# Optimization experiments

Measured on AMD Instinct MI355X. Metric: run time of the kernel, lower is better.

The kernel has to match this reference:

```python
import jax, jax.numpy as jnp
import numpy as np

B, S, D = 32, 1024, 512
MAX_DUR = 8  # randint upper bound; after clamp durations lie in [1, MAX_DUR-1]


def setup_inputs() -> dict:
    key = jax.random.key(0)
    kx, kd = jax.random.split(key)
    x = jax.random.normal(kx, (B, S, D), dtype=jnp.float32)
    durations = jax.random.randint(kd, (B, S), 0, MAX_DUR).astype(jnp.int64)
    return {"x": x, "durations": durations}


def reference(x, durations):
    # torch: durations.long().clamp(min=1); per-batch repeat_interleave then
    # pad_sequence to the max expanded length across the batch.
    dur = jnp.clip(durations.astype(jnp.int32), 1, None)          # [B,S]
    cum = jnp.cumsum(dur, axis=1)                                  # [B,S] exclusive-right boundaries
    totals = cum[:, -1]                                            # [B] expanded lengths
    # pad_sequence pads to max total length across the batch; this is
    # intrinsically data-dependent, so concretize it eagerly.
    max_len = int(jnp.max(totals))
    pos = jnp.arange(max_len)                                      # [T]
    # token index for output frame t: smallest s with cum[s] > t
    idx = jax.vmap(lambda c: jnp.searchsorted(c, pos, side='right'))(cum)  # [B,T]
    idx = jnp.minimum(idx, S - 1)
    out = jnp.take_along_axis(x, idx[:, :, None], axis=1)          # [B,T,D] fused gather
    mask = (pos[None, :] < totals[:, None]).astype(x.dtype)        # zero the ragged tail
    return out * mask[:, :, None]
```

## Files before the change

kernel.cpp:

```cpp
#include <hip/hip_runtime.h>
#include <hip/hip_bf16.h>


constexpr int B = 32;
constexpr int S = 1024;
constexpr int D = 512;
constexpr int VEC = D / 4;
constexpr int BPB = 64;
constexpr int MAX_RPB = 128;

using f4 = __attribute__((ext_vector_type(4))) float;

__global__ void lr_fused(const int* __restrict__ durations,
                         const f4* __restrict__ x4,
                         f4* __restrict__ out,
                         int max_len) {
    const int b   = blockIdx.x >> 6;
    const int blk = blockIdx.x & (BPB - 1);
    const int rpb = (max_len + BPB - 1) / BPB;
    const int p0  = blk * rpb;
    const int p1  = min(p0 + rpb, max_len);
    if (p0 >= p1) return;

    const int t    = threadIdx.x;
    const int lane = t & 63;
    const int wv   = t >> 6;

    __shared__ int wsum[4];
    __shared__ int s_idx[MAX_RPB];

    int4 d4 = reinterpret_cast<const int4*>(durations + b * S)[t];
    const int d0 = d4.x < 1 ? 1 : d4.x;
    const int d1 = d4.y < 1 ? 1 : d4.y;
    const int d2 = d4.z < 1 ? 1 : d4.z;
    const int d3 = d4.w < 1 ? 1 : d4.w;
    const int tsum = d0 + d1 + d2 + d3;

    int inc = tsum;
    #pragma unroll
    for (int off = 1; off < 64; off <<= 1) {
        int n = __shfl_up(inc, off, 64);
        if (lane >= off) inc += n;
    }
    if (lane == 63) wsum[wv] = inc;

    const int nblk = p1 - p0;
    for (int q = t; q < nblk; q += 256) s_idx[q] = -1;
    __syncthreads();

    int base = 0;
    #pragma unroll
    for (int j = 0; j < 4; ++j) if (j < wv) base += wsum[j];

    int p = base + inc - tsum;
    int src = b * S + t * 4;
    {
        int e;
        e = p + d0; for (int q = max(p, p0); q < min(e, p1); ++q) s_idx[q - p0] = src; p = e; ++src;
        e = p + d1; for (int q = max(p, p0); q < min(e, p1); ++q) s_idx[q - p0] = src; p = e; ++src;
        e = p + d2; for (int q = max(p, p0); q < min(e, p1); ++q) s_idx[q - p0] = src; p = e; ++src;
        e = p + d3; for (int q = max(p, p0); q < min(e, p1); ++q) s_idx[q - p0] = src;
    }
    __syncthreads();

    const int qr = (nblk + 3) >> 2;
    int r  = wv * qr;
    int r1 = min(r + qr, nblk);

    f4* __restrict__ dbase = out + ((size_t)b * max_len + p0) * VEC;

    for (; r + 4 <= r1; r += 4) {
        const int i0 = __builtin_amdgcn_readfirstlane(s_idx[r]);
        const int i1 = __builtin_amdgcn_readfirstlane(s_idx[r + 1]);
        const int i2 = __builtin_amdgcn_readfirstlane(s_idx[r + 2]);
        const int i3 = __builtin_amdgcn_readfirstlane(s_idx[r + 3]);

        f4 a0 = {0,0,0,0}, c0 = {0,0,0,0};
        f4 a1 = {0,0,0,0}, c1 = {0,0,0,0};
        f4 a2 = {0,0,0,0}, c2 = {0,0,0,0};
        f4 a3 = {0,0,0,0}, c3 = {0,0,0,0};
        if (i0 >= 0) { const f4* s = x4 + (size_t)i0 * VEC; a0 = s[lane]; c0 = s[lane + 64]; }
        if (i1 >= 0) { const f4* s = x4 + (size_t)i1 * VEC; a1 = s[lane]; c1 = s[lane + 64]; }
        if (i2 >= 0) { const f4* s = x4 + (size_t)i2 * VEC; a2 = s[lane]; c2 = s[lane + 64]; }
        if (i3 >= 0) { const f4* s = x4 + (size_t)i3 * VEC; a3 = s[lane]; c3 = s[lane + 64]; }

        f4* __restrict__ d = dbase + (size_t)r * VEC;
        __builtin_nontemporal_store(a0, d + lane);
        __builtin_nontemporal_store(c0, d + lane + 64);
        __builtin_nontemporal_store(a1, d + VEC + lane);
        __builtin_nontemporal_store(c1, d + VEC + lane + 64);
        __builtin_nontemporal_store(a2, d + 2 * VEC + lane);
        __builtin_nontemporal_store(c2, d + 2 * VEC + lane + 64);
        __builtin_nontemporal_store(a3, d + 3 * VEC + lane);
        __builtin_nontemporal_store(c3, d + 3 * VEC + lane + 64);
    }
    for (; r < r1; ++r) {
        const int i0 = __builtin_amdgcn_readfirstlane(s_idx[r]);
        f4 a = {0,0,0,0}, c = {0,0,0,0};
        if (i0 >= 0) { const f4* s = x4 + (size_t)i0 * VEC; a = s[lane]; c = s[lane + 64]; }
        f4* __restrict__ d = dbase + (size_t)r * VEC;
        __builtin_nontemporal_store(a, d + lane);
        __builtin_nontemporal_store(c, d + lane + 64);
    }
}

extern "C" void kernel_launch(void* const* d_in, const int* in_sizes, int n_in,
                              void* d_out, int out_size, void* d_ws, size_t ws_size,
                              hipStream_t stream) {
    const float* x = (const float*)d_in[0];
    const int* durations = (const int*)d_in[1];
    float* out = (float*)d_out;

    const int max_len = out_size / (B * D);

    lr_fused<<<B * BPB, 256, 0, stream>>>(
        durations, (const f4*)x, (f4*)out, max_len);
}
```

Measured before the change: 55.10 us.

## Use 1024-thread blocks with one token per thread and fewer blocks per batch

Blocks per batch drop from 64 to 16 and block size grows from 256 to 1024 threads. Each thread now scans a single duration instead of four, and sixteen waves split the gather rows. The change cuts the number of blocks that each redo the full 1024-token prefix scan, so less scan work is repeated per output row. In exchange blocks are larger and fewer (512 total), which may reduce latency hiding and adds a 16-wave cross-wave sum.

```diff
diff --git a/kernel.cpp b/kernel.cpp
--- a/kernel.cpp
+++ b/kernel.cpp
@@ -6,16 +6,18 @@
 constexpr int S = 1024;
 constexpr int D = 512;
 constexpr int VEC = D / 4;
-constexpr int BPB = 64;
-constexpr int MAX_RPB = 128;
+constexpr int BPB = 16;
+constexpr int NW  = 16;
+constexpr int MAX_RPB = 320;
 
 using f4 = __attribute__((ext_vector_type(4))) float;
 
-__global__ void lr_fused(const int* __restrict__ durations,
-                         const f4* __restrict__ x4,
-                         f4* __restrict__ out,
-                         int max_len) {
-    const int b   = blockIdx.x >> 6;
+__global__ __launch_bounds__(1024, 2)
+void lr_fused(const int* __restrict__ durations,
+              const f4* __restrict__ x4,
+              f4* __restrict__ out,
+              int max_len) {
+    const int b   = blockIdx.x >> 4;
     const int blk = blockIdx.x & (BPB - 1);
     const int rpb = (max_len + BPB - 1) / BPB;
     const int p0  = blk * rpb;
@@ -26,17 +28,13 @@
     const int lane = t & 63;
     const int wv   = t >> 6;
 
-    __shared__ int wsum[4];
+    __shared__ int wsum[NW];
     __shared__ int s_idx[MAX_RPB];
 
-    int4 d4 = reinterpret_cast<const int4*>(durations + b * S)[t];
-    const int d0 = d4.x < 1 ? 1 : d4.x;
-    const int d1 = d4.y < 1 ? 1 : d4.y;
-    const int d2 = d4.z < 1 ? 1 : d4.z;
-    const int d3 = d4.w < 1 ? 1 : d4.w;
-    const int tsum = d0 + d1 + d2 + d3;
+    int d = durations[b * S + t];
+    if (d < 1) d = 1;
 
-    int inc = tsum;
+    int inc = d;
     #pragma unroll
     for (int off = 1; off < 64; off <<= 1) {
         int n = __shfl_up(inc, off, 64);
@@ -45,25 +43,20 @@
     if (lane == 63) wsum[wv] = inc;
 
     const int nblk = p1 - p0;
-    for (int q = t; q < nblk; q += 256) s_idx[q] = -1;
+    for (int q = t; q < nblk; q += 1024) s_idx[q] = -1;
     __syncthreads();
 
     int base = 0;
     #pragma unroll
-    for (int j = 0; j < 4; ++j) if (j < wv) base += wsum[j];
+    for (int j = 0; j < NW; ++j) if (j < wv) base += wsum[j];
 
-    int p = base + inc - tsum;
-    int src = b * S + t * 4;
-    {
-        int e;
-        e = p + d0; for (int q = max(p, p0); q < min(e, p1); ++q) s_idx[q - p0] = src; p = e; ++src;
-        e = p + d1; for (int q = max(p, p0); q < min(e, p1); ++q) s_idx[q - p0] = src; p = e; ++src;
-        e = p + d2; for (int q = max(p, p0); q < min(e, p1); ++q) s_idx[q - p0] = src; p = e; ++src;
-        e = p + d3; for (int q = max(p, p0); q < min(e, p1); ++q) s_idx[q - p0] = src;
-    }
+    const int pstart = base + inc - d;
+    const int pend   = pstart + d;
+    const int src    = b * S + t;
+    for (int q = max(pstart, p0); q < min(pend, p1); ++q) s_idx[q - p0] = src;
     __syncthreads();
 
-    const int qr = (nblk + 3) >> 2;
+    const int qr = (nblk + NW - 1) / NW;
     int r  = wv * qr;
     int r1 = min(r + qr, nblk);
 
@@ -84,23 +77,23 @@
         if (i2 >= 0) { const f4* s = x4 + (size_t)i2 * VEC; a2 = s[lane]; c2 = s[lane + 64]; }
         if (i3 >= 0) { const f4* s = x4 + (size_t)i3 * VEC; a3 = s[lane]; c3 = s[lane + 64]; }
 
-        f4* __restrict__ d = dbase + (size_t)r * VEC;
-        __builtin_nontemporal_store(a0, d + lane);
-        __builtin_nontemporal_store(c0, d + lane + 64);
-        __builtin_nontemporal_store(a1, d + VEC + lane);
-        __builtin_nontemporal_store(c1, d + VEC + lane + 64);
-        __builtin_nontemporal_store(a2, d + 2 * VEC + lane);
-        __builtin_nontemporal_store(c2, d + 2 * VEC + lane + 64);
-        __builtin_nontemporal_store(a3, d + 3 * VEC + lane);
-        __builtin_nontemporal_store(c3, d + 3 * VEC + lane + 64);
+        f4* __restrict__ dst = dbase + (size_t)r * VEC;
+        __builtin_nontemporal_store(a0, dst + lane);
+        __builtin_nontemporal_store(c0, dst + lane + 64);
+        __builtin_nontemporal_store(a1, dst + VEC + lane);
+        __builtin_nontemporal_store(c1, dst + VEC + lane + 64);
+        __builtin_nontemporal_store(a2, dst + 2 * VEC + lane);
+        __builtin_nontemporal_store(c2, dst + 2 * VEC + lane + 64);
+        __builtin_nontemporal_store(a3, dst + 3 * VEC + lane);
+        __builtin_nontemporal_store(c3, dst + 3 * VEC + lane + 64);
     }
     for (; r < r1; ++r) {
         const int i0 = __builtin_amdgcn_readfirstlane(s_idx[r]);
         f4 a = {0,0,0,0}, c = {0,0,0,0};
         if (i0 >= 0) { const f4* s = x4 + (size_t)i0 * VEC; a = s[lane]; c = s[lane + 64]; }
-        f4* __restrict__ d = dbase + (size_t)r * VEC;
-        __builtin_nontemporal_store(a, d + lane);
-        __builtin_nontemporal_store(c, d + lane + 64);
+        f4* __restrict__ dst = dbase + (size_t)r * VEC;
+        __builtin_nontemporal_store(a, dst + lane);
+        __builtin_nontemporal_store(c, dst + lane + 64);
     }
 }
 
@@ -113,6 +106,6 @@
 
     const int max_len = out_size / (B * D);
 
-    lr_fused<<<B * BPB, 256, 0, stream>>>(
+    lr_fused<<<B * BPB, 1024, 0, stream>>>(
         durations, (const f4*)x, (f4*)out, max_len);
 }
```

New measurement: 53.40 us. 3.1% less time.
